# Performance work log

Hardware: AMD Instinct MI355X
Metric: run time of the kernel (lower is better)

## Reference

```python
import jax, jax.numpy as jnp
import numpy as np

IN, OUT, HID = 1024, 1024, 2048
L = IN + OUT + HID
EPS = 1e-12  # F.normalize default eps


def _make_strength_matrix():
    fwd_s, bwd_s, lat_s, self_s = 1.0, 0.5, 0.3, 0.0
    i = np.arange(L)
    # torch: triu (incl diag) = forward, then tril (incl diag) = backward -> diag ends up backward here
    A = np.where(i[:, None] >= i[None, :], bwd_s, fwd_s).astype(np.float32)
    # lateral blocks (within input, within output, within hidden)
    A[0:IN, 0:IN] = lat_s
    A[IN:IN + OUT, IN:IN + OUT] = lat_s
    A[IN + OUT:L, IN + OUT:L] = lat_s
    A[i, i] = self_s
    return A


def setup_inputs() -> dict:
    key = jax.random.key(0)
    kx, ky, kw = jax.random.split(key, 3)
    B = 1024
    x = jax.random.normal(kx, (B, IN), dtype=jnp.float32)
    y = jax.random.normal(ky, (B, OUT), dtype=jnp.float32)
    W = jax.random.normal(kw, (L, L), dtype=jnp.float32) * 0.01
    idx = jnp.arange(L)
    W = W.at[idx, idx].set(0.0)  # fill_diagonal_(0) at init
    A = jnp.asarray(_make_strength_matrix())
    return {"x": x, "y": y, "W": W, "A": A, "n": 32}


def reference(x, y, W, A, n):
    # clamp_x=True, clamp_y=False, norm_hidden=True, average_window<=0
    B = x.shape[0]
    act0 = jnp.concatenate(
        [x, jnp.zeros_like(y), jnp.zeros((B, HID), dtype=x.dtype)], axis=1
    )  # [B, L]
    mw = W * A.T  # modified weights, loop-invariant

    def step(act, _):
        act = jax.nn.relu(act @ mw.T)          # linear(act, mw) + relu
        act = act.at[:, :IN].set(x)            # clamp_x
        hid = act[:, IN + OUT:]
        nrm = jnp.linalg.norm(hid, axis=1, keepdims=True)
        hid = hid / jnp.maximum(nrm, EPS)      # F.normalize p=2 dim=1
        act = act.at[:, IN + OUT:].set(hid)
        return act, None

    act, _ = jax.lax.scan(step, act0, None, length=n)
    return act
```

## Files before the change

kernel.cpp:

```cpp
#include <hip/hip_runtime.h>
#include <stdint.h>
#include <stddef.h>


#define L 4096
#define INX 1024
#define OUTX 1024
#define BATCH 1024
#define NCOL 3072
#define NITER 32

#define BM 64
#define BN 96
#define BK 64

typedef float floatx4 __attribute__((ext_vector_type(4)));
typedef short bf16x8 __attribute__((ext_vector_type(8)));

__device__ __forceinline__ unsigned short f2bf(float f) {
  unsigned int u = __float_as_uint(f);
  u += 0x7FFF + ((u >> 16) & 1);
  return (unsigned short)(u >> 16);
}
__device__ __forceinline__ float bf2f(unsigned short h) {
  return __uint_as_float(((unsigned int)h) << 16);
}

__device__ __forceinline__ void load_lds_16B(const void* g, void* s) {
  __builtin_amdgcn_global_load_lds(
      (const __attribute__((address_space(1))) unsigned int*)g,
      (__attribute__((address_space(3))) unsigned int*)s, 16, 0, 0);
}

__global__ void prep_mwn(const float* __restrict__ W, unsigned short* __restrict__ mwn) {
  int idx = blockIdx.x * 256 + threadIdx.x;
  int i = idx >> 10;
  int j4 = (idx & 1023) << 2;
  const float4 w = *(const float4*)&W[(size_t)(INX + i) * L + j4];
  const int c = INX + i;
  const int rc = (c < 2048) ? 1 : 2;
  float wv[4] = {w.x, w.y, w.z, w.w};
  unsigned short o[4];
#pragma unroll
  for (int k = 0; k < 4; ++k) {
    int j = j4 + k;
    int rj = (j < 1024) ? 0 : ((j < 2048) ? 1 : 2);
    float a = (j == c) ? 0.0f : ((rj == rc) ? 0.3f : ((j >= c) ? 0.5f : 1.0f));
    o[k] = f2bf(wv[k] * a);
  }
  *(ushort4*)&mwn[(size_t)i * L + j4] = make_ushort4(o[0], o[1], o[2], o[3]);
}

__global__ void init_act(const float* __restrict__ x, unsigned short* __restrict__ actA) {
  int i = blockIdx.x * 256 + threadIdx.x;
  int col = i & (L - 1), row = i >> 12;
  actA[i] = (col < INX) ? f2bf(x[(size_t)row * INX + col]) : (unsigned short)0;
}

__device__ __forceinline__ void stage(unsigned short* As, unsigned short* Bs,
                                      const unsigned short* gA, const unsigned short* gB,
                                      int kb, int t) {
  const int srow = t >> 3, schunk = t & 7;
  const int o = srow * BK + schunk * 8;
  load_lds_16B(gA + kb, &As[o]);
  load_lds_16B(gA + (size_t)32 * L + kb, &As[o + 32 * BK]);
  load_lds_16B(gB + kb, &Bs[o]);
  load_lds_16B(gB + (size_t)32 * L + kb, &Bs[o + 32 * BK]);
  load_lds_16B(gB + (size_t)64 * L + kb, &Bs[o + 64 * BK]);
}

__device__ __forceinline__ void mfma_step(const unsigned short* As, const unsigned short* Bs,
                                          int wm, int wn, int l15, int quad,
                                          floatx4 acc[2][3]) {
#pragma unroll
  for (int kk = 0; kk < 2; ++kk) {
    bf16x8 af[2], bfr[3];
    const int c = kk * 4 + quad;
#pragma unroll
    for (int mt = 0; mt < 2; ++mt) {
      int r = wm + mt * 16 + l15;
      af[mt] = *(const bf16x8*)&As[r * BK + ((c ^ (r & 7)) * 8)];
    }
#pragma unroll
    for (int nt = 0; nt < 3; ++nt) {
      int r = wn + nt * 16 + l15;
      bfr[nt] = *(const bf16x8*)&Bs[r * BK + ((c ^ (r & 7)) * 8)];
    }
#pragma unroll
    for (int mt = 0; mt < 2; ++mt)
#pragma unroll
      for (int nt = 0; nt < 3; ++nt)
        acc[mt][nt] = __builtin_amdgcn_mfma_f32_16x16x32_bf16(af[mt], bfr[nt],
                                                              acc[mt][nt], 0, 0, 0);
  }
}

#define PSTEP(s, R, D, ACC)                                                       \
  do {                                                                            \
    if ((s) < NS - 1) asm volatile("s_waitcnt vmcnt(5)" ::: "memory");            \
    else              asm volatile("s_waitcnt vmcnt(0)" ::: "memory");            \
    asm volatile("s_barrier" ::: "memory");                                       \
    if ((s) + 2 < NS) stage(As##D, Bs##D, gA, gB, KB0 + ((s) + 2) * BK, t);       \
    mfma_step(As##R, Bs##R, wm, wn, l15, quad, ACC);                              \
  } while (0)

template<int MODE>
__global__ __launch_bounds__(256, 2) void gemm_k(
    const unsigned short* __restrict__ act,
    const unsigned short* __restrict__ mwn,
    unsigned short* __restrict__ actn,
    unsigned short* __restrict__ c0,
    const float* __restrict__ nsq_prev,
    float* __restrict__ nsq_next) {
  __shared__ alignas(16) unsigned short As0[BM * BK], As1[BM * BK], As2[BM * BK];
  __shared__ alignas(16) unsigned short Bs0[BN * BK], Bs1[BN * BK], Bs2[BN * BK];
  const int t = threadIdx.x;
  const int lane = t & 63;
  const int wave = t >> 6;
  const int wm = (wave & 1) * 32;
  const int wn = (wave >> 1) * 48;
  const int l15 = lane & 15;
  const int quad = lane >> 4;

  const int b = blockIdx.y * 32 + blockIdx.x;
  const int n_idx = (b & 7) * 4 + (b >> 7);
  const int m_idx = (b >> 3) & 15;
  const int m0 = m_idx * BM;
  const int n0 = n_idx * BN;

  const int srow = t >> 3;
  const int schunk = t & 7;
  const int gchunk = schunk ^ (srow & 7);
  const unsigned short* gA = act + (size_t)(m0 + srow) * L + gchunk * 8;
  const unsigned short* gB = mwn + (size_t)(n0 + srow) * L + gchunk * 8;

  const int KB0 = MODE ? INX : 0;
  constexpr int NS = MODE ? 48 : 16;

  floatx4 accA[2][3], accB[2][3];
#pragma unroll
  for (int i = 0; i < 2; ++i)
#pragma unroll
    for (int j = 0; j < 3; ++j) {
      accA[i][j] = (floatx4){0.f, 0.f, 0.f, 0.f};
      if (MODE) accB[i][j] = (floatx4){0.f, 0.f, 0.f, 0.f};
    }

  stage(As0, Bs0, gA, gB, KB0, t);
  stage(As1, Bs1, gA, gB, KB0 + BK, t);

  PSTEP(0, 0, 2, accA);  PSTEP(1, 1, 0, accA);  PSTEP(2, 2, 1, accA);
  PSTEP(3, 0, 2, accA);  PSTEP(4, 1, 0, accA);  PSTEP(5, 2, 1, accA);
  PSTEP(6, 0, 2, accA);  PSTEP(7, 1, 0, accA);  PSTEP(8, 2, 1, accA);
  PSTEP(9, 0, 2, accA);  PSTEP(10, 1, 0, accA); PSTEP(11, 2, 1, accA);
  PSTEP(12, 0, 2, accA); PSTEP(13, 1, 0, accA); PSTEP(14, 2, 1, accA);
  PSTEP(15, 0, 2, accA);
  if (MODE) {
    PSTEP(16, 1, 0, accB); PSTEP(17, 2, 1, accB); PSTEP(18, 0, 2, accB);
    PSTEP(19, 1, 0, accB); PSTEP(20, 2, 1, accB); PSTEP(21, 0, 2, accB);
    PSTEP(22, 1, 0, accB); PSTEP(23, 2, 1, accB); PSTEP(24, 0, 2, accB);
    PSTEP(25, 1, 0, accB); PSTEP(26, 2, 1, accB); PSTEP(27, 0, 2, accB);
    PSTEP(28, 1, 0, accB); PSTEP(29, 2, 1, accB); PSTEP(30, 0, 2, accB);
    PSTEP(31, 1, 0, accB); PSTEP(32, 2, 1, accB); PSTEP(33, 0, 2, accB);
    PSTEP(34, 1, 0, accB); PSTEP(35, 2, 1, accB); PSTEP(36, 0, 2, accB);
    PSTEP(37, 1, 0, accB); PSTEP(38, 2, 1, accB); PSTEP(39, 0, 2, accB);
    PSTEP(40, 1, 0, accB); PSTEP(41, 2, 1, accB); PSTEP(42, 0, 2, accB);
    PSTEP(43, 1, 0, accB); PSTEP(44, 2, 1, accB); PSTEP(45, 0, 2, accB);
    PSTEP(46, 1, 0, accB); PSTEP(47, 2, 1, accB);
  }

  if (MODE == 0) {
#pragma unroll
    for (int mt = 0; mt < 2; ++mt)
#pragma unroll
      for (int nt = 0; nt < 3; ++nt) {
        const int gn = n0 + wn + nt * 16 + l15;
#pragma unroll
        for (int r = 0; r < 4; ++r) {
          const int gm = m0 + wm + mt * 16 + quad * 4 + r;
          c0[(size_t)gm * NCOL + gn] = f2bf(accA[mt][nt][r]);
        }
      }
    return;
  }

  float sm[2][4];
#pragma unroll
  for (int mt = 0; mt < 2; ++mt)
#pragma unroll
    for (int r = 0; r < 4; ++r) {
      const int gm = m0 + wm + mt * 16 + quad * 4 + r;
      sm[mt][r] = 1.0f / fmaxf(sqrtf(nsq_prev[gm]), 1e-12f);
    }

  const bool has_hid = (n0 + BN) > OUTX;
#pragma unroll
  for (int mt = 0; mt < 2; ++mt) {
    float ss[4] = {0.f, 0.f, 0.f, 0.f};
#pragma unroll
    for (int nt = 0; nt < 3; ++nt) {
      const int gn = n0 + wn + nt * 16 + l15;
      const bool hid = gn >= OUTX;
#pragma unroll
      for (int r = 0; r < 4; ++r) {
        const int gm = m0 + wm + mt * 16 + quad * 4 + r;
        float v = bf2f(c0[(size_t)gm * NCOL + gn]) + accA[mt][nt][r]
                  + sm[mt][r] * accB[mt][nt][r];
        v = fmaxf(v, 0.f);
        actn[(size_t)gm * L + INX + gn] = f2bf(v);
        if (hid) ss[r] += v * v;
      }
    }
    if (has_hid) {
#pragma unroll
      for (int r = 0; r < 4; ++r) {
        float sv = ss[r];
        sv += __shfl_xor(sv, 1);
        sv += __shfl_xor(sv, 2);
        sv += __shfl_xor(sv, 4);
        sv += __shfl_xor(sv, 8);
        if (l15 == 0)
          atomicAdd(&nsq_next[m0 + wm + mt * 16 + quad * 4 + r], sv);
      }
    }
  }
}

__global__ void finalize(const float* __restrict__ x, const unsigned short* __restrict__ act,
                         const float* __restrict__ nsq_fin, float* __restrict__ out) {
  int i = blockIdx.x * 256 + threadIdx.x;
  int col = i & (L - 1), row = i >> 12;
  float v;
  if (col < INX) {
    v = x[(size_t)row * INX + col];
  } else {
    v = bf2f(act[i]);
    if (col >= INX + OUTX) v *= 1.0f / fmaxf(sqrtf(nsq_fin[row]), 1e-12f);
  }
  out[i] = v;
}

extern "C" void kernel_launch(void* const* d_in, const int* in_sizes, int n_in,
                              void* d_out, int out_size, void* d_ws, size_t ws_size,
                              hipStream_t stream) {
  const float* x = (const float*)d_in[0];
  const float* W = (const float*)d_in[2];
  float* out = (float*)d_out;

  char* ws = (char*)d_ws;
  unsigned short* mwn  = (unsigned short*)(ws);
  unsigned short* actA = (unsigned short*)(ws + 25165824);
  unsigned short* actB = (unsigned short*)(ws + 33554432);
  unsigned short* c0   = (unsigned short*)(ws + 41943040);
  float* normsq        = (float*)(ws + 48234496);

  hipMemsetAsync(normsq, 0, (NITER + 1) * BATCH * sizeof(float), stream);
  prep_mwn<<<(NCOL * (L / 4)) / 256, 256, 0, stream>>>(W, mwn);
  init_act<<<(BATCH * L) / 256, 256, 0, stream>>>(x, actA);

  gemm_k<0><<<dim3(NCOL / BN, BATCH / BM), 256, 0, stream>>>(actA, mwn, nullptr, c0,
                                                             nullptr, nullptr);

  unsigned short* cur = actA;
  unsigned short* nxt = actB;
  for (int it = 0; it < NITER; ++it) {
    gemm_k<1><<<dim3(NCOL / BN, BATCH / BM), 256, 0, stream>>>(
        cur, mwn, nxt, c0, normsq + it * BATCH, normsq + (it + 1) * BATCH);
    unsigned short* tmp = cur; cur = nxt; nxt = tmp;
  }
  finalize<<<(BATCH * L) / 256, 256, 0, stream>>>(x, cur, normsq + NITER * BATCH, out);
}
```

Baseline: 1.093 ms.

## Load A fragments directly from global into registers and pack c0 per-thread

The A operand (activations) is no longer staged through LDS. Each wave loads its bf16 MFMA fragments straight from global memory into double-buffered registers one step ahead, while only B keeps the triple-buffered LDS pipeline, and the wait count is adjusted to match. The c0 partial result is now stored and reloaded in a per-thread contiguous packed layout with 16-byte vector accesses instead of scattered 2-byte stores. This cuts LDS traffic and shared memory use and makes the c0 round trip coalesced, at the cost of more VGPRs and uncoalesced global fragment loads whose latency the pipeline must hide.

Result: slower. 2.009 ms (+83.8%).

```diff
diff --git a/kernel.cpp b/kernel.cpp
--- a/kernel.cpp
+++ b/kernel.cpp
@@ -57,30 +57,33 @@
   actA[i] = (col < INX) ? f2bf(x[(size_t)row * INX + col]) : (unsigned short)0;
 }
 
-__device__ __forceinline__ void stage(unsigned short* As, unsigned short* Bs,
-                                      const unsigned short* gA, const unsigned short* gB,
+__device__ __forceinline__ void stage(unsigned short* Bs, const unsigned short* gB,
                                       int kb, int t) {
   const int srow = t >> 3, schunk = t & 7;
   const int o = srow * BK + schunk * 8;
-  load_lds_16B(gA + kb, &As[o]);
-  load_lds_16B(gA + (size_t)32 * L + kb, &As[o + 32 * BK]);
   load_lds_16B(gB + kb, &Bs[o]);
   load_lds_16B(gB + (size_t)32 * L + kb, &Bs[o + 32 * BK]);
   load_lds_16B(gB + (size_t)64 * L + kb, &Bs[o + 64 * BK]);
 }
 
-__device__ __forceinline__ void mfma_step(const unsigned short* As, const unsigned short* Bs,
-                                          int wm, int wn, int l15, int quad,
+__device__ __forceinline__ void afrag_load(bf16x8 (&dst)[2][2],
+                                           const unsigned short* g0,
+                                           const unsigned short* g1, int kb) {
+#pragma unroll
+  for (int kk = 0; kk < 2; ++kk) {
+    dst[0][kk] = *(const bf16x8*)&g0[kb + kk * 32];
+    dst[1][kk] = *(const bf16x8*)&g1[kb + kk * 32];
+  }
+}
+
+__device__ __forceinline__ void mfma_step(const unsigned short* Bs,
+                                          const bf16x8 (&af)[2][2],
+                                          int wn, int l15, int quad,
                                           floatx4 acc[2][3]) {
 #pragma unroll
   for (int kk = 0; kk < 2; ++kk) {
-    bf16x8 af[2], bfr[3];
+    bf16x8 bfr[3];
     const int c = kk * 4 + quad;
-#pragma unroll
-    for (int mt = 0; mt < 2; ++mt) {
-      int r = wm + mt * 16 + l15;
-      af[mt] = *(const bf16x8*)&As[r * BK + ((c ^ (r & 7)) * 8)];
-    }
 #pragma unroll
     for (int nt = 0; nt < 3; ++nt) {
       int r = wn + nt * 16 + l15;
@@ -90,18 +93,22 @@
     for (int mt = 0; mt < 2; ++mt)
 #pragma unroll
       for (int nt = 0; nt < 3; ++nt)
-        acc[mt][nt] = __builtin_amdgcn_mfma_f32_16x16x32_bf16(af[mt], bfr[nt],
+        acc[mt][nt] = __builtin_amdgcn_mfma_f32_16x16x32_bf16(af[mt][kk], bfr[nt],
                                                               acc[mt][nt], 0, 0, 0);
   }
 }
 
 #define PSTEP(s, R, D, ACC)                                                       \
   do {                                                                            \
-    if ((s) < NS - 1) asm volatile("s_waitcnt vmcnt(5)" ::: "memory");            \
+    if ((s) < NS - 1) asm volatile("s_waitcnt vmcnt(3)" ::: "memory");            \
     else              asm volatile("s_waitcnt vmcnt(0)" ::: "memory");            \
     asm volatile("s_barrier" ::: "memory");                                       \
-    if ((s) + 2 < NS) stage(As##D, Bs##D, gA, gB, KB0 + ((s) + 2) * BK, t);       \
-    mfma_step(As##R, Bs##R, wm, wn, l15, quad, ACC);                              \
+    if ((s) + 1 < NS)                                                             \
+      afrag_load(afr[((s) + 1) & 1], gA0, gA1, KB0 + ((s) + 1) * BK);             \
+    asm volatile("" ::: "memory");                                                \
+    if ((s) + 2 < NS) stage(Bs##D, gB, KB0 + ((s) + 2) * BK, t);                  \
+    asm volatile("" ::: "memory");                                                \
+    mfma_step(Bs##R, afr[(s) & 1], wn, l15, quad, ACC);                           \
   } while (0)
 
 template<int MODE>
@@ -112,7 +119,6 @@
     unsigned short* __restrict__ c0,
     const float* __restrict__ nsq_prev,
     float* __restrict__ nsq_next) {
-  __shared__ alignas(16) unsigned short As0[BM * BK], As1[BM * BK], As2[BM * BK];
   __shared__ alignas(16) unsigned short Bs0[BN * BK], Bs1[BN * BK], Bs2[BN * BK];
   const int t = threadIdx.x;
   const int lane = t & 63;
@@ -131,8 +137,10 @@
   const int srow = t >> 3;
   const int schunk = t & 7;
   const int gchunk = schunk ^ (srow & 7);
-  const unsigned short* gA = act + (size_t)(m0 + srow) * L + gchunk * 8;
   const unsigned short* gB = mwn + (size_t)(n0 + srow) * L + gchunk * 8;
+
+  const unsigned short* gA0 = act + (size_t)(m0 + wm + l15) * L + quad * 8;
+  const unsigned short* gA1 = gA0 + (size_t)16 * L;
 
   const int KB0 = MODE ? INX : 0;
   constexpr int NS = MODE ? 48 : 16;
@@ -146,8 +154,14 @@
       if (MODE) accB[i][j] = (floatx4){0.f, 0.f, 0.f, 0.f};
     }
 
-  stage(As0, Bs0, gA, gB, KB0, t);
-  stage(As1, Bs1, gA, gB, KB0 + BK, t);
+  bf16x8 afr[2][2][2];
+
+  stage(Bs0, gB, KB0, t);
+  asm volatile("" ::: "memory");
+  afrag_load(afr[0], gA0, gA1, KB0);
+  asm volatile("" ::: "memory");
+  stage(Bs1, gB, KB0 + BK, t);
+  asm volatile("" ::: "memory");
 
   PSTEP(0, 0, 2, accA);  PSTEP(1, 1, 0, accA);  PSTEP(2, 2, 1, accA);
   PSTEP(3, 0, 2, accA);  PSTEP(4, 1, 0, accA);  PSTEP(5, 2, 1, accA);
@@ -170,18 +184,27 @@
   }
 
   if (MODE == 0) {
+    alignas(16) unsigned short buf[24];
 #pragma unroll
     for (int mt = 0; mt < 2; ++mt)
 #pragma unroll
-      for (int nt = 0; nt < 3; ++nt) {
-        const int gn = n0 + wn + nt * 16 + l15;
-#pragma unroll
-        for (int r = 0; r < 4; ++r) {
-          const int gm = m0 + wm + mt * 16 + quad * 4 + r;
-          c0[(size_t)gm * NCOL + gn] = f2bf(accA[mt][nt][r]);
-        }
-      }
+      for (int nt = 0; nt < 3; ++nt)
+#pragma unroll
+        for (int r = 0; r < 4; ++r)
+          buf[mt * 12 + nt * 4 + r] = f2bf(accA[mt][nt][r]);
+    unsigned short* p = c0 + ((size_t)b * 256 + t) * 24;
+    *(bf16x8*)&p[0]  = *(const bf16x8*)&buf[0];
+    *(bf16x8*)&p[8]  = *(const bf16x8*)&buf[8];
+    *(bf16x8*)&p[16] = *(const bf16x8*)&buf[16];
     return;
+  }
+
+  alignas(16) unsigned short c0s[24];
+  {
+    const unsigned short* p = c0 + ((size_t)b * 256 + t) * 24;
+    *(bf16x8*)&c0s[0]  = *(const bf16x8*)&p[0];
+    *(bf16x8*)&c0s[8]  = *(const bf16x8*)&p[8];
+    *(bf16x8*)&c0s[16] = *(const bf16x8*)&p[16];
   }
 
   float sm[2][4];
@@ -204,7 +227,7 @@
 #pragma unroll
       for (int r = 0; r < 4; ++r) {
         const int gm = m0 + wm + mt * 16 + quad * 4 + r;
-        float v = bf2f(c0[(size_t)gm * NCOL + gn]) + accA[mt][nt][r]
+        float v = bf2f(c0s[mt * 12 + nt * 4 + r]) + accA[mt][nt][r]
                   + sm[mt][r] * accB[mt][nt][r];
         v = fmaxf(v, 0.f);
         actn[(size_t)gm * L + INX + gn] = f2bf(v);
```

## Double GEMM M-tile to 128 with one block per CU and fragment-ordered c0

Applied to the files above, without the earlier changes.

Increases the block tile from 64x96 to 128x96, so the grid drops from 512 to 256 blocks (about one per CU), and each wave now computes a 64x48 sub-tile. This raises operand reuse from LDS and halves the number of blocks that re-stream W. The c0 partial product is stored in per-thread fragment order as contiguous 16-byte writes instead of strided scalar writes. The costs are higher register pressure (occupancy hint drops to 1 block), dynamic LDS of about 84 KB, and fewer blocks left to hide latency.

Result: no change. 1.108 ms (+1.4%).

```diff
diff --git a/kernel.cpp b/kernel.cpp
--- a/kernel.cpp
+++ b/kernel.cpp
@@ -10,9 +10,10 @@
 #define NCOL 3072
 #define NITER 32
 
-#define BM 64
+#define BM 128
 #define BN 96
 #define BK 64
+#define SMEM_BYTES 86016
 
 typedef float floatx4 __attribute__((ext_vector_type(4)));
 typedef short bf16x8 __attribute__((ext_vector_type(8)));
@@ -64,6 +65,8 @@
   const int o = srow * BK + schunk * 8;
   load_lds_16B(gA + kb, &As[o]);
   load_lds_16B(gA + (size_t)32 * L + kb, &As[o + 32 * BK]);
+  load_lds_16B(gA + (size_t)64 * L + kb, &As[o + 64 * BK]);
+  load_lds_16B(gA + (size_t)96 * L + kb, &As[o + 96 * BK]);
   load_lds_16B(gB + kb, &Bs[o]);
   load_lds_16B(gB + (size_t)32 * L + kb, &Bs[o + 32 * BK]);
   load_lds_16B(gB + (size_t)64 * L + kb, &Bs[o + 64 * BK]);
@@ -71,13 +74,13 @@
 
 __device__ __forceinline__ void mfma_step(const unsigned short* As, const unsigned short* Bs,
                                           int wm, int wn, int l15, int quad,
-                                          floatx4 acc[2][3]) {
+                                          floatx4 acc[4][3]) {
 #pragma unroll
   for (int kk = 0; kk < 2; ++kk) {
-    bf16x8 af[2], bfr[3];
+    bf16x8 af[4], bfr[3];
     const int c = kk * 4 + quad;
 #pragma unroll
-    for (int mt = 0; mt < 2; ++mt) {
+    for (int mt = 0; mt < 4; ++mt) {
       int r = wm + mt * 16 + l15;
       af[mt] = *(const bf16x8*)&As[r * BK + ((c ^ (r & 7)) * 8)];
     }
@@ -87,7 +90,7 @@
       bfr[nt] = *(const bf16x8*)&Bs[r * BK + ((c ^ (r & 7)) * 8)];
     }
 #pragma unroll
-    for (int mt = 0; mt < 2; ++mt)
+    for (int mt = 0; mt < 4; ++mt)
 #pragma unroll
       for (int nt = 0; nt < 3; ++nt)
         acc[mt][nt] = __builtin_amdgcn_mfma_f32_16x16x32_bf16(af[mt], bfr[nt],
@@ -97,7 +100,7 @@
 
 #define PSTEP(s, R, D, ACC)                                                       \
   do {                                                                            \
-    if ((s) < NS - 1) asm volatile("s_waitcnt vmcnt(5)" ::: "memory");            \
+    if ((s) < NS - 1) asm volatile("s_waitcnt vmcnt(7)" ::: "memory");            \
     else              asm volatile("s_waitcnt vmcnt(0)" ::: "memory");            \
     asm volatile("s_barrier" ::: "memory");                                       \
     if ((s) + 2 < NS) stage(As##D, Bs##D, gA, gB, KB0 + ((s) + 2) * BK, t);       \
@@ -105,26 +108,32 @@
   } while (0)
 
 template<int MODE>
-__global__ __launch_bounds__(256, 2) void gemm_k(
+__global__ __launch_bounds__(256, 1) void gemm_k(
     const unsigned short* __restrict__ act,
     const unsigned short* __restrict__ mwn,
     unsigned short* __restrict__ actn,
     unsigned short* __restrict__ c0,
     const float* __restrict__ nsq_prev,
     float* __restrict__ nsq_next) {
-  __shared__ alignas(16) unsigned short As0[BM * BK], As1[BM * BK], As2[BM * BK];
-  __shared__ alignas(16) unsigned short Bs0[BN * BK], Bs1[BN * BK], Bs2[BN * BK];
+  extern __shared__ unsigned short smem[];
+  unsigned short* const As0 = smem;
+  unsigned short* const As1 = smem + 8192;
+  unsigned short* const As2 = smem + 16384;
+  unsigned short* const Bs0 = smem + 24576;
+  unsigned short* const Bs1 = smem + 30720;
+  unsigned short* const Bs2 = smem + 36864;
+
   const int t = threadIdx.x;
   const int lane = t & 63;
   const int wave = t >> 6;
-  const int wm = (wave & 1) * 32;
-  const int wn = (wave >> 1) * 48;
+  const int wm = (wave >> 1) * 64;
+  const int wn = (wave & 1) * 48;
   const int l15 = lane & 15;
   const int quad = lane >> 4;
 
   const int b = blockIdx.y * 32 + blockIdx.x;
-  const int n_idx = (b & 7) * 4 + (b >> 7);
-  const int m_idx = (b >> 3) & 15;
+  const int m_idx = b & 7;
+  const int n_idx = b >> 3;
   const int m0 = m_idx * BM;
   const int n0 = n_idx * BN;
 
@@ -137,9 +146,9 @@
   const int KB0 = MODE ? INX : 0;
   constexpr int NS = MODE ? 48 : 16;
 
-  floatx4 accA[2][3], accB[2][3];
-#pragma unroll
-  for (int i = 0; i < 2; ++i)
+  floatx4 accA[4][3], accB[4][3];
+#pragma unroll
+  for (int i = 0; i < 4; ++i)
 #pragma unroll
     for (int j = 0; j < 3; ++j) {
       accA[i][j] = (floatx4){0.f, 0.f, 0.f, 0.f};
@@ -170,32 +179,41 @@
   }
 
   if (MODE == 0) {
-#pragma unroll
-    for (int mt = 0; mt < 2; ++mt)
-#pragma unroll
-      for (int nt = 0; nt < 3; ++nt) {
-        const int gn = n0 + wn + nt * 16 + l15;
-#pragma unroll
-        for (int r = 0; r < 4; ++r) {
-          const int gm = m0 + wm + mt * 16 + quad * 4 + r;
-          c0[(size_t)gm * NCOL + gn] = f2bf(accA[mt][nt][r]);
-        }
-      }
+    alignas(16) unsigned short buf[48];
+#pragma unroll
+    for (int mt = 0; mt < 4; ++mt)
+#pragma unroll
+      for (int nt = 0; nt < 3; ++nt)
+#pragma unroll
+        for (int r = 0; r < 4; ++r)
+          buf[mt * 12 + nt * 4 + r] = f2bf(accA[mt][nt][r]);
+    unsigned short* p = c0 + ((size_t)b * 256 + t) * 48;
+#pragma unroll
+    for (int k = 0; k < 6; ++k)
+      *(bf16x8*)&p[k * 8] = *(const bf16x8*)&buf[k * 8];
     return;
   }
 
-  float sm[2][4];
-#pragma unroll
-  for (int mt = 0; mt < 2; ++mt)
+  alignas(16) unsigned short c0s[48];
+  {
+    const unsigned short* p = c0 + ((size_t)b * 256 + t) * 48;
+#pragma unroll
+    for (int k = 0; k < 6; ++k)
+      *(bf16x8*)&c0s[k * 8] = *(const bf16x8*)&p[k * 8];
+  }
+
+  float sm[4][4];
+#pragma unroll
+  for (int mt = 0; mt < 4; ++mt)
 #pragma unroll
     for (int r = 0; r < 4; ++r) {
       const int gm = m0 + wm + mt * 16 + quad * 4 + r;
       sm[mt][r] = 1.0f / fmaxf(sqrtf(nsq_prev[gm]), 1e-12f);
     }
 
-  const bool has_hid = (n0 + BN) > OUTX;
-#pragma unroll
-  for (int mt = 0; mt < 2; ++mt) {
+  const bool has_hid = (n0 + wn + 48) > OUTX;
+#pragma unroll
+  for (int mt = 0; mt < 4; ++mt) {
     float ss[4] = {0.f, 0.f, 0.f, 0.f};
 #pragma unroll
     for (int nt = 0; nt < 3; ++nt) {
@@ -204,7 +222,7 @@
 #pragma unroll
       for (int r = 0; r < 4; ++r) {
         const int gm = m0 + wm + mt * 16 + quad * 4 + r;
-        float v = bf2f(c0[(size_t)gm * NCOL + gn]) + accA[mt][nt][r]
+        float v = bf2f(c0s[mt * 12 + nt * 4 + r]) + accA[mt][nt][r]
                   + sm[mt][r] * accB[mt][nt][r];
         v = fmaxf(v, 0.f);
         actn[(size_t)gm * L + INX + gn] = f2bf(v);
@@ -254,17 +272,26 @@
   unsigned short* c0   = (unsigned short*)(ws + 41943040);
   float* normsq        = (float*)(ws + 48234496);
 
+  static bool attr_done = false;
+  if (!attr_done) {
+    (void)hipFuncSetAttribute(reinterpret_cast<const void*>(&gemm_k<0>),
+                              hipFuncAttributeMaxDynamicSharedMemorySize, SMEM_BYTES);
+    (void)hipFuncSetAttribute(reinterpret_cast<const void*>(&gemm_k<1>),
+                              hipFuncAttributeMaxDynamicSharedMemorySize, SMEM_BYTES);
+    attr_done = true;
+  }
+
   hipMemsetAsync(normsq, 0, (NITER + 1) * BATCH * sizeof(float), stream);
   prep_mwn<<<(NCOL * (L / 4)) / 256, 256, 0, stream>>>(W, mwn);
   init_act<<<(BATCH * L) / 256, 256, 0, stream>>>(x, actA);
 
-  gemm_k<0><<<dim3(NCOL / BN, BATCH / BM), 256, 0, stream>>>(actA, mwn, nullptr, c0,
-                                                             nullptr, nullptr);
+  gemm_k<0><<<dim3(32, 8), 256, SMEM_BYTES, stream>>>(actA, mwn, nullptr, c0,
+                                                      nullptr, nullptr);
 
   unsigned short* cur = actA;
   unsigned short* nxt = actB;
   for (int it = 0; it < NITER; ++it) {
-    gemm_k<1><<<dim3(NCOL / BN, BATCH / BM), 256, 0, stream>>>(
+    gemm_k<1><<<dim3(32, 8), 256, SMEM_BYTES, stream>>>(
         cur, mwn, nxt, c0, normsq + it * BATCH, normsq + (it + 1) * BATCH);
     unsigned short* tmp = cur; cur = nxt; nxt = tmp;
   }
```
